# Optimization experiments

Hardware: AMD Instinct MI355X
Metric: run time of the kernel (lower is better)

The kernel has to match this reference:

```python
import jax, jax.numpy as jnp
import numpy as np

NEW_INDEX = jnp.array([7, 0, 1, 6, 8, 2, 5, 4, 3], dtype=jnp.int32)
B, S, D, PF, LF, A = 65536, 20000, 300, 12, 8, 8
IN_DIM = PF + LF + 1  # 21
NCHW = ('NCHW', 'OIHW', 'NCHW')


def setup_inputs() -> dict:
    key = jax.random.key(0)
    ks = jax.random.split(key, 18)
    state = jax.random.randint(ks[0], (B,), 0, S)
    des = jax.random.randint(ks[1], (B,), 0, D)
    act = jax.random.randint(ks[2], (B,), 0, A)
    action_state_pad = jnp.concatenate(
        [jax.random.randint(ks[3], (S, A), 0, S), jnp.arange(S)[:, None]], axis=1)
    policy_mask_pad = jnp.concatenate(
        [jax.random.randint(ks[4], (S, A), 0, 2), jnp.zeros((S, 1), jnp.int32)], axis=1)
    path_feature = jax.random.normal(ks[5], (S, D, PF), jnp.float32)
    link_feature = jax.random.normal(ks[6], (S, LF), jnp.float32)
    w = lambda k, shp: jax.random.normal(k, shp, jnp.float32) * 0.05
    return {
        'state': state, 'des': des, 'act': act,
        'action_state_pad': action_state_pad, 'policy_mask_pad': policy_mask_pad,
        'path_feature': path_feature, 'link_feature': link_feature,
        'conv1_w': w(ks[7], (20, IN_DIM, 3, 3)), 'conv1_b': w(ks[8], (20,)),
        'conv2_w': w(ks[9], (30, 20, 2, 2)), 'conv2_b': w(ks[10], (30,)),
        'fc1_w': w(ks[11], (120, 30 + A)), 'fc1_b': w(ks[12], (120,)),
        'fc2_w': w(ks[13], (84, 120)), 'fc2_b': w(ks[14], (84,)),
        'fc3_w': w(ks[15], (1, 84)), 'fc3_b': w(ks[16], (1,)),
    }


def _process_features(state, des, action_state_pad, policy_mask_pad, path_feature, link_feature):
    neigh = action_state_pad[state]                       # [B, 9]
    npf = path_feature[neigh, des[:, None], :]            # [B, 9, PF]
    nef = link_feature[neigh]                             # [B, 9, LF]
    nmf = policy_mask_pad[state][..., None].astype(npf.dtype)  # [B, 9, 1]
    feat = jnp.concatenate([npf, nef, nmf], axis=-1)[:, NEW_INDEX, :]  # [B, 9, 21]
    x = feat.reshape(feat.shape[0], 3, 3, -1)             # [B, 3, 3, 21]
    return x.transpose(0, 3, 1, 2)                        # [B, 21, 3, 3]


def reference(state, des, act, action_state_pad, policy_mask_pad, path_feature,
              link_feature, conv1_w, conv1_b, conv2_w, conv2_b,
              fc1_w, fc1_b, fc2_w, fc2_b, fc3_w, fc3_b):
    lrelu = lambda v: jax.nn.leaky_relu(v, 0.2)
    x = _process_features(state, des, action_state_pad, policy_mask_pad,
                          path_feature, link_feature)
    x = jax.lax.conv_general_dilated(x, conv1_w, (1, 1), ((1, 1), (1, 1)),
                                     dimension_numbers=NCHW) + conv1_b[:, None, None]
    x = lrelu(x)                                          # [B, 20, 3, 3]
    x = jax.lax.reduce_window(x, -jnp.inf, jax.lax.max,
                              (1, 1, 2, 2), (1, 1, 1, 1), 'VALID')  # [B, 20, 2, 2]
    x = jax.lax.conv_general_dilated(x, conv2_w, (1, 1), 'VALID',
                                     dimension_numbers=NCHW) + conv2_b[:, None, None]
    x = lrelu(x).reshape(-1, 30)                          # [B, 30]
    x = jnp.concatenate([x, jax.nn.one_hot(act, A, dtype=x.dtype)], axis=1)  # [B, 38]
    x = lrelu(x @ fc1_w.T + fc1_b)
    x = lrelu(x @ fc2_w.T + fc2_b)
    return jax.nn.sigmoid(x @ fc3_w.T + fc3_b)            # [B, 1]
```

## Files before the change

kernel.cpp:

```cpp
#include <hip/hip_runtime.h>
#include <hip/hip_bf16.h>
#include <math.h>

#define DDIM   300
#define PFN    12
#define LFN    8
#define ICH    21
#define TPB    384
#define SPB    96
#define SLOT_DW 99
#define W1P    1980
#define W2P    1200
#define FW1H   2280
#define FW2H   5040

__device__ __forceinline__ float lrelu(float v) { return v > 0.0f ? v : 0.2f * v; }

__device__ __forceinline__ unsigned int pack2(float a, float b) {
    union { __hip_bfloat162 h; unsigned int u; } cv;
    cv.h.x = __float2bfloat16(a);
    cv.h.y = __float2bfloat16(b);
    return cv.u;
}
__device__ __forceinline__ float bflo(unsigned int u) {
    union { unsigned int i; float f; } c; c.i = u << 16; return c.f;
}
__device__ __forceinline__ float bfhi(unsigned int u) {
    union { unsigned int i; float f; } c; c.i = u & 0xffff0000u; return c.f;
}

__device__ __forceinline__ float dot2bf(unsigned int a, unsigned int b, float c) {
    float d;
    asm("v_dot2_f32_bf16 %0, %1, %2, %3" : "=v"(d) : "v"(a), "v"(b), "v"(c));
    return d;
}

__device__ __forceinline__ void conv_acc2(float o[9], const unsigned int w[9],
                                          const unsigned int fv[9]) {
#pragma unroll
    for (int t = 0; t < 9; ++t) {
        const int ky = t / 3 - 1, kx = t % 3 - 1;
        const unsigned int wv = w[t];
#pragma unroll
        for (int y = 0; y < 3; ++y) {
            const int iy = y + ky;
            if (iy < 0 || iy > 2) continue;
#pragma unroll
            for (int x = 0; x < 3; ++x) {
                const int ix = x + kx;
                if (ix < 0 || ix > 2) continue;
                o[y * 3 + x] = dot2bf(wv, fv[iy * 3 + ix], o[y * 3 + x]);
            }
        }
    }
}

__launch_bounds__(TPB, 3)
__global__ void disc_kernel(
    const int* __restrict__ state, const int* __restrict__ des,
    const int* __restrict__ act,
    const int* __restrict__ asp_g,
    const int* __restrict__ pmp_g,
    const float* __restrict__ path_feature,
    const float* __restrict__ link_feature,
    const float* __restrict__ w1, const float* __restrict__ b1,
    const float* __restrict__ w2, const float* __restrict__ b2,
    const float* __restrict__ fw1, const float* __restrict__ fb1,
    const float* __restrict__ fw2, const float* __restrict__ fb2,
    const float* __restrict__ fw3, const float* __restrict__ fb3,
    float* __restrict__ out, int n)
{
    __shared__ __align__(16) unsigned int w1p[W1P];
    __shared__ __align__(16) unsigned int w2p[W2P];
    __shared__ __align__(16) unsigned int fw1h[FW1H];
    __shared__ __align__(16) unsigned int fw2h[FW2H];
    __shared__ unsigned int feat[SPB * SLOT_DW];

    const int tid = threadIdx.x;

    {
        for (int i = tid; i < W1P; i += TPB) {
            const int oc = i / 99, r = i % 99, icp = r / 9, t = r % 9;
            const float lo = w1[(oc * ICH + 2 * icp) * 9 + t];
            const float hi = (icp < 10) ? w1[(oc * ICH + 2 * icp + 1) * 9 + t] : 0.0f;
            w1p[i] = pack2(lo, hi);
        }
        for (int i = tid; i < W2P; i += TPB) {
            const int j = i / 40, r = i % 40, oc = r / 2, h = r % 2;
            w2p[i] = pack2(w2[j * 80 + oc * 4 + 2 * h], w2[j * 80 + oc * 4 + 2 * h + 1]);
        }
        const float2* sf1 = (const float2*)fw1;
        for (int i = tid; i < FW1H; i += TPB) { const float2 v = sf1[i]; fw1h[i] = pack2(v.x, v.y); }
        const float2* sf2 = (const float2*)fw2;
        for (int i = tid; i < FW2H; i += TPB) { const float2 v = sf2[i]; fw2h[i] = pack2(v.x, v.y); }
    }
    __syncthreads();

    const int lane4  = tid & 3;
    const int lsamp  = tid >> 2;
    const int sample = blockIdx.x * SPB + lsamp;
    if (sample >= n) return;

    const int s  = state[sample];
    const int d  = des[sample];
    const int ai = act[sample];

    const int* asp = asp_g + s * 9;
    const int* pmp = pmp_g + s * 9;
    unsigned int* fslot = feat + lsamp * SLOT_DW;

#pragma unroll
    for (int t = 0; t < 3; ++t) {
        const int p = lane4 + 4 * t;
        if (p < 9) {
            const int a  = (int)((0x345286107ULL >> (4 * p)) & 0xF);
            const int na = asp[a];
            const float m = (float)pmp[a];
            const float4* pf = (const float4*)(path_feature + (na * DDIM + d) * PFN);
            const float4 v0 = pf[0], v1 = pf[1], v2 = pf[2];
            const float4* lf = (const float4*)(link_feature + na * LFN);
            const float4 u0 = lf[0], u1 = lf[1];
            unsigned int* dst = fslot + p * 11;
            dst[0] = pack2(v0.x, v0.y); dst[1] = pack2(v0.z, v0.w);
            dst[2] = pack2(v1.x, v1.y); dst[3] = pack2(v1.z, v1.w);
            dst[4] = pack2(v2.x, v2.y); dst[5] = pack2(v2.z, v2.w);
            dst[6] = pack2(u0.x, u0.y); dst[7] = pack2(u0.z, u0.w);
            dst[8] = pack2(u1.x, u1.y); dst[9] = pack2(u1.z, u1.w);
            dst[10] = pack2(m, 0.0f);
        }
    }
    asm volatile("s_waitcnt lgkmcnt(0)" ::: "memory");

    const int oc0 = lane4 * 5;
    float o[5][9];
#pragma unroll
    for (int c = 0; c < 5; ++c) {
        const float bb = b1[oc0 + c];
#pragma unroll
        for (int q = 0; q < 9; ++q) o[c][q] = bb;
    }

#pragma unroll 1
    for (int icp = 0; icp < 11; ++icp) {
        unsigned int fwd[9];
#pragma unroll
        for (int q = 0; q < 9; ++q) fwd[q] = fslot[q * 11 + icp];
        unsigned int wt[9];
#pragma unroll
        for (int c = 0; c < 5; ++c) {
            const unsigned int* wrow = w1p + (oc0 + c) * 99 + icp * 9;
#pragma unroll
            for (int t = 0; t < 9; ++t) wt[t] = wrow[t];
            conv_acc2(o[c], wt, fwd);
        }
    }

    unsigned int pp[5][2];
#pragma unroll
    for (int c = 0; c < 5; ++c) {
        float v[9];
#pragma unroll
        for (int q = 0; q < 9; ++q) v[q] = lrelu(o[c][q]);
        const float p0 = fmaxf(fmaxf(v[0], v[1]), fmaxf(v[3], v[4]));
        const float p1 = fmaxf(fmaxf(v[1], v[2]), fmaxf(v[4], v[5]));
        const float p2 = fmaxf(fmaxf(v[3], v[4]), fmaxf(v[6], v[7]));
        const float p3 = fmaxf(fmaxf(v[4], v[5]), fmaxf(v[7], v[8]));
        pp[c][0] = pack2(p0, p1);
        pp[c][1] = pack2(p2, p3);
    }

    float x30[30];
#pragma unroll
    for (int j = 0; j < 30; ++j) {
        const unsigned int* wb = w2p + j * 40 + oc0 * 2;
        float acc = 0.0f;
#pragma unroll
        for (int c = 0; c < 5; ++c) {
            acc = dot2bf(wb[2 * c],     pp[c][0], acc);
            acc = dot2bf(wb[2 * c + 1], pp[c][1], acc);
        }
        acc += __shfl_xor(acc, 1, 64);
        acc += __shfl_xor(acc, 2, 64);
        x30[j] = lrelu(acc + b2[j]);
    }

    unsigned int xp[15];
#pragma unroll
    for (int m = 0; m < 15; ++m) xp[m] = pack2(x30[2 * m], x30[2 * m + 1]);

    float h1[30];
    const int j0 = lane4 * 30;
    const int ohd   = (30 + ai) >> 1;
    const int ohodd = (30 + ai) & 1;
#pragma unroll
    for (int jj = 0; jj < 30; ++jj) {
        const unsigned int* wr = fw1h + (j0 + jj) * 19;
        const unsigned int uoh = wr[ohd];
        float acc = fb1[j0 + jj] + (ohodd ? bfhi(uoh) : bflo(uoh));
#pragma unroll
        for (int m = 0; m < 15; ++m)
            acc = dot2bf(wr[m], xp[m], acc);
        h1[jj] = lrelu(acc);
    }

    unsigned int hp[15];
#pragma unroll
    for (int m = 0; m < 15; ++m) hp[m] = pack2(h1[2 * m], h1[2 * m + 1]);

    float z = fb3[0];
#pragma unroll 2
    for (int i = 0; i < 84; ++i) {
        const unsigned int* wp = fw2h + i * 60 + lane4 * 15;
        float a = 0.0f;
#pragma unroll
        for (int m = 0; m < 15; ++m)
            a = dot2bf(wp[m], hp[m], a);
        a += __shfl_xor(a, 1, 64);
        a += __shfl_xor(a, 2, 64);
        z = fmaf(fw3[i], lrelu(a + fb2[i]), z);
    }

    if (lane4 == 0)
        out[sample] = 1.0f / (1.0f + __expf(-z));
}

extern "C" void kernel_launch(void* const* d_in, const int* in_sizes, int n_in,
                              void* d_out, int out_size, void* d_ws, size_t ws_size,
                              hipStream_t stream) {
    const int*   state = (const int*)d_in[0];
    const int*   des   = (const int*)d_in[1];
    const int*   act   = (const int*)d_in[2];
    const int*   asp   = (const int*)d_in[3];
    const int*   pmp   = (const int*)d_in[4];
    const float* pathf = (const float*)d_in[5];
    const float* linkf = (const float*)d_in[6];
    const float* w1    = (const float*)d_in[7];
    const float* b1    = (const float*)d_in[8];
    const float* w2    = (const float*)d_in[9];
    const float* b2    = (const float*)d_in[10];
    const float* fw1   = (const float*)d_in[11];
    const float* fb1   = (const float*)d_in[12];
    const float* fw2   = (const float*)d_in[13];
    const float* fb2   = (const float*)d_in[14];
    const float* fw3   = (const float*)d_in[15];
    const float* fb3   = (const float*)d_in[16];

    const int n = in_sizes[0];
    dim3 grid((n + SPB - 1) / SPB), block(TPB);
    hipLaunchKernelGGL(disc_kernel, grid, block, 0, stream,
                       state, des, act, asp, pmp, pathf, linkf,
                       w1, b1, w2, b2, fw1, fb1, fw2, fb2, fw3, fb3,
                       (float*)d_out, n);
}
```

Before: 491.6 us.

## Pad shared weight and feature layouts for 128-bit LDS loads and bigger blocks

Re-lays out the conv1 weights (tap-major with input-channel pairs padded to 12), the feature slots (padded to 12 dwords) and the FC weight rows (padded to 20) so that shared-memory reads become uint4/uint2 vector loads. The conv1 loop is fully unrolled over three channel groups. fc2 uses two accumulators to shorten the dependency chain. The block grows to 1024 threads (256 samples) with two blocks per CU, which amortises the weight staging but raises LDS use per block and register pressure from the full unroll.

```diff
diff --git a/kernel.cpp b/kernel.cpp
--- a/kernel.cpp
+++ b/kernel.cpp
@@ -6,13 +6,13 @@
 #define PFN    12
 #define LFN    8
 #define ICH    21
-#define TPB    384
-#define SPB    96
-#define SLOT_DW 99
-#define W1P    1980
+#define TPB    1024
+#define SPB    256
+#define SLOT_DW 108
+#define W1Q    2160
 #define W2P    1200
-#define FW1H   2280
-#define FW2H   5040
+#define FW1P   2400
+#define FW2P   6720
 
 __device__ __forceinline__ float lrelu(float v) { return v > 0.0f ? v : 0.2f * v; }
 
@@ -35,27 +35,7 @@
     return d;
 }
 
-__device__ __forceinline__ void conv_acc2(float o[9], const unsigned int w[9],
-                                          const unsigned int fv[9]) {
-#pragma unroll
-    for (int t = 0; t < 9; ++t) {
-        const int ky = t / 3 - 1, kx = t % 3 - 1;
-        const unsigned int wv = w[t];
-#pragma unroll
-        for (int y = 0; y < 3; ++y) {
-            const int iy = y + ky;
-            if (iy < 0 || iy > 2) continue;
-#pragma unroll
-            for (int x = 0; x < 3; ++x) {
-                const int ix = x + kx;
-                if (ix < 0 || ix > 2) continue;
-                o[y * 3 + x] = dot2bf(wv, fv[iy * 3 + ix], o[y * 3 + x]);
-            }
-        }
-    }
-}
-
-__launch_bounds__(TPB, 3)
+__launch_bounds__(TPB, 2)
 __global__ void disc_kernel(
     const int* __restrict__ state, const int* __restrict__ des,
     const int* __restrict__ act,
@@ -70,29 +50,42 @@
     const float* __restrict__ fw3, const float* __restrict__ fb3,
     float* __restrict__ out, int n)
 {
-    __shared__ __align__(16) unsigned int w1p[W1P];
+    __shared__ __align__(16) unsigned int w1q[W1Q];
     __shared__ __align__(16) unsigned int w2p[W2P];
-    __shared__ __align__(16) unsigned int fw1h[FW1H];
-    __shared__ __align__(16) unsigned int fw2h[FW2H];
-    __shared__ unsigned int feat[SPB * SLOT_DW];
+    __shared__ __align__(16) unsigned int fw1h[FW1P];
+    __shared__ __align__(16) unsigned int fw2h[FW2P];
+    __shared__ __align__(16) unsigned int feat[SPB * SLOT_DW];
 
     const int tid = threadIdx.x;
 
     {
-        for (int i = tid; i < W1P; i += TPB) {
-            const int oc = i / 99, r = i % 99, icp = r / 9, t = r % 9;
-            const float lo = w1[(oc * ICH + 2 * icp) * 9 + t];
-            const float hi = (icp < 10) ? w1[(oc * ICH + 2 * icp + 1) * 9 + t] : 0.0f;
-            w1p[i] = pack2(lo, hi);
+        for (int i = tid; i < W1Q; i += TPB) {
+            const int oc = i / 108, r = i % 108, t = r / 12, icp = r % 12;
+            unsigned int v = 0u;
+            if (icp < 11) {
+                const float lo = w1[(oc * ICH + 2 * icp) * 9 + t];
+                const float hi = (icp < 10) ? w1[(oc * ICH + 2 * icp + 1) * 9 + t] : 0.0f;
+                v = pack2(lo, hi);
+            }
+            w1q[i] = v;
         }
         for (int i = tid; i < W2P; i += TPB) {
             const int j = i / 40, r = i % 40, oc = r / 2, h = r % 2;
             w2p[i] = pack2(w2[j * 80 + oc * 4 + 2 * h], w2[j * 80 + oc * 4 + 2 * h + 1]);
         }
-        const float2* sf1 = (const float2*)fw1;
-        for (int i = tid; i < FW1H; i += TPB) { const float2 v = sf1[i]; fw1h[i] = pack2(v.x, v.y); }
-        const float2* sf2 = (const float2*)fw2;
-        for (int i = tid; i < FW2H; i += TPB) { const float2 v = sf2[i]; fw2h[i] = pack2(v.x, v.y); }
+        for (int i = tid; i < FW1P; i += TPB) {
+            const int row = i / 20, col = i % 20;
+            unsigned int v = 0u;
+            if (col < 19) v = pack2(fw1[row * 38 + 2 * col], fw1[row * 38 + 2 * col + 1]);
+            fw1h[i] = v;
+        }
+        for (int i = tid; i < FW2P; i += TPB) {
+            const int row = i / 80, c = i % 80, ch = c / 20, m = c % 20;
+            unsigned int v = 0u;
+            if (m < 15) v = pack2(fw2[row * 120 + ch * 30 + 2 * m],
+                                  fw2[row * 120 + ch * 30 + 2 * m + 1]);
+            fw2h[i] = v;
+        }
     }
     __syncthreads();
 
@@ -120,7 +113,7 @@
             const float4 v0 = pf[0], v1 = pf[1], v2 = pf[2];
             const float4* lf = (const float4*)(link_feature + na * LFN);
             const float4 u0 = lf[0], u1 = lf[1];
-            unsigned int* dst = fslot + p * 11;
+            unsigned int* dst = fslot + p * 12;
             dst[0] = pack2(v0.x, v0.y); dst[1] = pack2(v0.z, v0.w);
             dst[2] = pack2(v1.x, v1.y); dst[3] = pack2(v1.z, v1.w);
             dst[4] = pack2(v2.x, v2.y); dst[5] = pack2(v2.z, v2.w);
@@ -140,18 +133,40 @@
         for (int q = 0; q < 9; ++q) o[c][q] = bb;
     }
 
-#pragma unroll 1
-    for (int icp = 0; icp < 11; ++icp) {
-        unsigned int fwd[9];
-#pragma unroll
-        for (int q = 0; q < 9; ++q) fwd[q] = fslot[q * 11 + icp];
-        unsigned int wt[9];
+#pragma unroll
+    for (int g = 0; g < 3; ++g) {
+        uint4 f4[9];
+#pragma unroll
+        for (int q = 0; q < 9; ++q)
+            f4[q] = *(const uint4*)(fslot + q * 12 + 4 * g);
 #pragma unroll
         for (int c = 0; c < 5; ++c) {
-            const unsigned int* wrow = w1p + (oc0 + c) * 99 + icp * 9;
-#pragma unroll
-            for (int t = 0; t < 9; ++t) wt[t] = wrow[t];
-            conv_acc2(o[c], wt, fwd);
+            const uint4* wrow = (const uint4*)(w1q + (oc0 + c) * 108) + g;
+#pragma unroll
+            for (int t = 0; t < 9; ++t) {
+                const uint4 w4 = wrow[t * 3];
+                const int ky = t / 3 - 1, kx = t % 3 - 1;
+#pragma unroll
+                for (int ic = 0; ic < 4; ++ic) {
+                    if (g == 2 && ic == 3) continue;
+                    const unsigned int wv =
+                        (ic == 0) ? w4.x : (ic == 1) ? w4.y : (ic == 2) ? w4.z : w4.w;
+#pragma unroll
+                    for (int y = 0; y < 3; ++y) {
+                        const int iy = y + ky;
+                        if (iy < 0 || iy > 2) continue;
+#pragma unroll
+                        for (int x = 0; x < 3; ++x) {
+                            const int ix = x + kx;
+                            if (ix < 0 || ix > 2) continue;
+                            const uint4 fq = f4[iy * 3 + ix];
+                            const unsigned int fv =
+                                (ic == 0) ? fq.x : (ic == 1) ? fq.y : (ic == 2) ? fq.z : fq.w;
+                            o[c][y * 3 + x] = dot2bf(wv, fv, o[c][y * 3 + x]);
+                        }
+                    }
+                }
+            }
         }
     }
 
@@ -172,12 +187,13 @@
     float x30[30];
 #pragma unroll
     for (int j = 0; j < 30; ++j) {
-        const unsigned int* wb = w2p + j * 40 + oc0 * 2;
+        const uint2* wb = (const uint2*)(w2p + j * 40 + oc0 * 2);
         float acc = 0.0f;
 #pragma unroll
         for (int c = 0; c < 5; ++c) {
-            acc = dot2bf(wb[2 * c],     pp[c][0], acc);
-            acc = dot2bf(wb[2 * c + 1], pp[c][1], acc);
+            const uint2 w = wb[c];
+            acc = dot2bf(w.x, pp[c][0], acc);
+            acc = dot2bf(w.y, pp[c][1], acc);
         }
         acc += __shfl_xor(acc, 1, 64);
         acc += __shfl_xor(acc, 2, 64);
@@ -194,12 +210,17 @@
     const int ohodd = (30 + ai) & 1;
 #pragma unroll
     for (int jj = 0; jj < 30; ++jj) {
-        const unsigned int* wr = fw1h + (j0 + jj) * 19;
+        const unsigned int* wr = fw1h + (j0 + jj) * 20;
+        const uint4* w4p = (const uint4*)wr;
+        const uint4 a0 = w4p[0], a1 = w4p[1], a2 = w4p[2];
+        const unsigned int w12 = wr[12], w13 = wr[13], w14 = wr[14];
         const unsigned int uoh = wr[ohd];
         float acc = fb1[j0 + jj] + (ohodd ? bfhi(uoh) : bflo(uoh));
+        const unsigned int wv[15] = {a0.x, a0.y, a0.z, a0.w, a1.x, a1.y, a1.z, a1.w,
+                                     a2.x, a2.y, a2.z, a2.w, w12, w13, w14};
 #pragma unroll
         for (int m = 0; m < 15; ++m)
-            acc = dot2bf(wr[m], xp[m], acc);
+            acc = dot2bf(wv[m], xp[m], acc);
         h1[jj] = lrelu(acc);
     }
 
@@ -210,11 +231,18 @@
     float z = fb3[0];
 #pragma unroll 2
     for (int i = 0; i < 84; ++i) {
-        const unsigned int* wp = fw2h + i * 60 + lane4 * 15;
-        float a = 0.0f;
-#pragma unroll
-        for (int m = 0; m < 15; ++m)
-            a = dot2bf(wp[m], hp[m], a);
+        const uint4* w4 = (const uint4*)(fw2h + i * 80 + lane4 * 20);
+        const uint4 a0 = w4[0], a1 = w4[1], a2 = w4[2], a3 = w4[3];
+        float alo = 0.0f, ahi = 0.0f;
+        alo = dot2bf(a0.x, hp[0],  alo);  ahi = dot2bf(a2.x, hp[8],  ahi);
+        alo = dot2bf(a0.y, hp[1],  alo);  ahi = dot2bf(a2.y, hp[9],  ahi);
+        alo = dot2bf(a0.z, hp[2],  alo);  ahi = dot2bf(a2.z, hp[10], ahi);
+        alo = dot2bf(a0.w, hp[3],  alo);  ahi = dot2bf(a2.w, hp[11], ahi);
+        alo = dot2bf(a1.x, hp[4],  alo);  ahi = dot2bf(a3.x, hp[12], ahi);
+        alo = dot2bf(a1.y, hp[5],  alo);  ahi = dot2bf(a3.y, hp[13], ahi);
+        alo = dot2bf(a1.z, hp[6],  alo);  ahi = dot2bf(a3.z, hp[14], ahi);
+        alo = dot2bf(a1.w, hp[7],  alo);
+        float a = alo + ahi;
         a += __shfl_xor(a, 1, 64);
         a += __shfl_xor(a, 2, 64);
         z = fmaf(fw3[i], lrelu(a + fb2[i]), z);
```

After: 430.7 us. -12.4%, faster.
